# Kernel tuning notes

Measured on AMD Instinct MI355X. Metric: run time of the kernel, lower is better.

Reference implementation:

```python
import jax, jax.numpy as jnp
import numpy as np

VOCAB = 32000
HID = 1024
LAYERS = 2
BATCH = 16
SEQ = 256


def setup_inputs() -> dict:
    key = jax.random.key(0)
    ks = jax.random.split(key, 8)
    s = 1.0 / np.sqrt(HID)
    x = jax.random.randint(ks[0], (BATCH, SEQ), 0, VOCAB, dtype=jnp.int64)
    embed = jax.random.normal(ks[1], (VOCAB, HID), dtype=jnp.float32) * 0.02
    Wi = jax.random.uniform(ks[2], (LAYERS, HID, HID), jnp.float32, -s, s)
    bi = jax.random.uniform(ks[3], (LAYERS, HID), jnp.float32, -s, s)
    Wh = jax.random.uniform(ks[4], (LAYERS, HID, HID), jnp.float32, -s, s)
    bh = jax.random.uniform(ks[5], (LAYERS, HID), jnp.float32, -s, s)
    Wo = jax.random.uniform(ks[6], (VOCAB, HID), jnp.float32, -s, s)
    bo = jax.random.uniform(ks[7], (VOCAB,), jnp.float32, -s, s)
    return {"x": x, "embed": embed, "Wi": Wi, "bi": bi, "Wh": Wh, "bh": bh, "Wo": Wo, "bo": bo}


def reference(x, embed, Wi, bi, Wh, bh, Wo, bo):
    B, S = x.shape
    L, H, _ = Wi.shape
    emb = embed[x]                      # [B, S, H]
    emb_t = jnp.swapaxes(emb, 0, 1)     # [S, B, H]
    h0 = jnp.zeros((L, B, H), dtype=embed.dtype)

    def step(hidden, x_t):
        inp = x_t
        new_h = []
        for l in range(L):
            inp = jnp.tanh(inp @ Wi[l].T + bi[l] + hidden[l] @ Wh[l].T + bh[l])
            new_h.append(inp)
        hidden = jnp.stack(new_h)       # [L, B, H]
        return hidden, inp              # emit top-layer hidden per step

    hidden, tops = jax.lax.scan(step, h0, emb_t)   # tops: [S, B, H]
    # project all steps at once (same math as per-step fc_out)
    logits = jnp.einsum('sbh,vh->bsv', tops, Wo) + bo  # [B, S, V]
    return logits, hidden
```

## Files before the change

kernel.cpp:

```cpp
#include <hip/hip_runtime.h>
#include <cmath>
#include <cstdint>

#define VOCAB 32000
#define HID   1024
#define BATCH 16
#define SEQ   256
#define NL0   64
#define NL1   128
#define MASTER 192
#define NBLK  256
#define BH    (BATCH * HID)
#define NTILE_M 16
#define NTILE_N 125
#define NTILES  (NTILE_M * NTILE_N)

typedef __attribute__((ext_vector_type(8))) short short8;
typedef __attribute__((ext_vector_type(4))) float f32x4;

__device__ __forceinline__ ushort f2bf(float f) {
  uint u = __builtin_bit_cast(uint, f);
  return (ushort)((u + 0x7FFFu + ((u >> 16) & 1u)) >> 16);
}
__device__ __forceinline__ float bf2f(ushort h) {
  return __builtin_bit_cast(float, (uint)h << 16);
}

#define LOAD8(d, base)                                                        \
  asm volatile(                                                               \
    "global_load_dwordx4 %0, %8, off sc0 sc1\n\t"                             \
    "global_load_dwordx4 %1, %8, off offset:512 sc0 sc1\n\t"                  \
    "global_load_dwordx4 %2, %8, off offset:1024 sc0 sc1\n\t"                 \
    "global_load_dwordx4 %3, %8, off offset:1536 sc0 sc1\n\t"                 \
    "global_load_dwordx4 %4, %8, off offset:2048 sc0 sc1\n\t"                 \
    "global_load_dwordx4 %5, %8, off offset:2560 sc0 sc1\n\t"                 \
    "global_load_dwordx4 %6, %8, off offset:3072 sc0 sc1\n\t"                 \
    "global_load_dwordx4 %7, %8, off offset:3584 sc0 sc1"                     \
    : "=&v"(d[0]), "=&v"(d[1]), "=&v"(d[2]), "=&v"(d[3]),                     \
      "=&v"(d[4]), "=&v"(d[5]), "=&v"(d[6]), "=&v"(d[7])                      \
    : "v"(base) : "memory")

#define WAIT8(d)                                                              \
  asm volatile("s_waitcnt vmcnt(0)"                                           \
    : "+v"(d[0]), "+v"(d[1]), "+v"(d[2]), "+v"(d[3]),                         \
      "+v"(d[4]), "+v"(d[5]), "+v"(d[6]), "+v"(d[7]) :: "memory")

__device__ __forceinline__ void st_coherent(float* p, float v) {
  asm volatile("global_store_dword %0, %1, off sc0 sc1" :: "v"(p), "v"(v) : "memory");
}
__device__ __forceinline__ int ld_rlx(const int* p) {
  return __hip_atomic_load(p, __ATOMIC_RELAXED, __HIP_MEMORY_SCOPE_AGENT);
}
__device__ __forceinline__ void st_rlx(int* p, int v) {
  __hip_atomic_store(p, v, __ATOMIC_RELAXED, __HIP_MEMORY_SCOPE_AGENT);
}

__global__ __launch_bounds__(256) void pre0_gemm(
    const int* __restrict__ x, const float* __restrict__ embed,
    const float* __restrict__ Wi0, const float* __restrict__ bi0,
    const float* __restrict__ bh0, float* __restrict__ pre)
{
  __shared__ float As[32][132];
  __shared__ float Bs[32][132];
  const int tid  = threadIdx.x;
  const int n0   = blockIdx.x * 128;
  const int m0   = blockIdx.y * 128;
  const int lrow = tid >> 3, lkq = tid & 7;
  const int ty   = tid >> 4, tx  = tid & 15;

  const float* arow[4];
#pragma unroll
  for (int q = 0; q < 4; ++q) {
    int m = m0 + lrow + 32 * q;
    int t = m >> 4, b = m & 15;
    arow[q] = embed + (size_t)x[b * SEQ + t] * HID;
  }
  const float* brow = Wi0 + (size_t)(n0 + lrow) * HID;

  float acc[8][8];
#pragma unroll
  for (int i = 0; i < 8; ++i)
#pragma unroll
    for (int j = 0; j < 8; ++j) acc[i][j] = 0.f;

  for (int kt = 0; kt < HID; kt += 32) {
    float4 av[4], bv[4];
#pragma unroll
    for (int q = 0; q < 4; ++q) {
      av[q] = *(const float4*)(arow[q] + kt + lkq * 4);
      bv[q] = *(const float4*)(brow + (size_t)(32 * q) * HID + kt + lkq * 4);
    }
    __syncthreads();
#pragma unroll
    for (int q = 0; q < 4; ++q) {
      int r = lrow + 32 * q;
      As[lkq*4+0][r] = av[q].x; As[lkq*4+1][r] = av[q].y;
      As[lkq*4+2][r] = av[q].z; As[lkq*4+3][r] = av[q].w;
      Bs[lkq*4+0][r] = bv[q].x; Bs[lkq*4+1][r] = bv[q].y;
      Bs[lkq*4+2][r] = bv[q].z; Bs[lkq*4+3][r] = bv[q].w;
    }
    __syncthreads();
#pragma unroll
    for (int kk = 0; kk < 32; ++kk) {
      float4 a0 = *(const float4*)&As[kk][ty * 8];
      float4 a1 = *(const float4*)&As[kk][ty * 8 + 4];
      float4 b0 = *(const float4*)&Bs[kk][tx * 8];
      float4 b1 = *(const float4*)&Bs[kk][tx * 8 + 4];
      float a[8] = {a0.x,a0.y,a0.z,a0.w,a1.x,a1.y,a1.z,a1.w};
      float b[8] = {b0.x,b0.y,b0.z,b0.w,b1.x,b1.y,b1.z,b1.w};
#pragma unroll
      for (int i = 0; i < 8; ++i)
#pragma unroll
        for (int j = 0; j < 8; ++j) acc[i][j] = fmaf(a[i], b[j], acc[i][j]);
    }
  }

#pragma unroll
  for (int i = 0; i < 8; ++i) {
    int m = m0 + ty * 8 + i;
    float* o = pre + (size_t)m * HID + n0 + tx * 8;
#pragma unroll
    for (int j = 0; j < 8; ++j) {
      int n = n0 + tx * 8 + j;
      o[j] = acc[i][j] + bi0[n] + bh0[n];
    }
  }
}

__global__ __launch_bounds__(512) void rnn_scan(
    const float* __restrict__ Wi, const float* __restrict__ Wh,
    const float* __restrict__ bi, const float* __restrict__ bh,
    const float* __restrict__ pre0, float* __restrict__ h0ring,
    float* __restrict__ h1g, float* __restrict__ tops,
    const float* __restrict__ Wo, const float* __restrict__ bo,
    float* __restrict__ out, int* __restrict__ bar)
{
  __shared__ __align__(16) char pool[139328];
  __shared__ int tkt_s;
  const int tid = threadIdx.x;
  const int blk = blockIdx.x;
  int* go0    = bar + 12 * 32;
  int* go1    = bar + 13 * 32;
  int* ticket = bar + 14 * 32;

  auto proj_tiles = [&]() {
    ushort* Ahi = (ushort*)pool;
    ushort* Alo = Ahi + 16384;
    ushort* Bs  = Alo + 16384;
    const int lane = tid & 63, wv = tid >> 6;
    const int wm = wv & 3, wn = wv >> 2;
    const int sr = tid >> 4;
    const int sk = (tid & 15) * 4;
    for (;;) {
      if (tid == 0)
        tkt_s = __hip_atomic_fetch_add(ticket, 1, __ATOMIC_RELAXED,
                                       __HIP_MEMORY_SCOPE_AGENT);
      __syncthreads();
      const int T = tkt_s;
      if (T >= NTILES) break;
      const int mt = T / NTILE_N, nt = T % NTILE_N;
      if (tid == 0) {
        int need = 16 * (mt + 1); if (need > SEQ) need = SEQ;
        while (ld_rlx(go1) < need) __builtin_amdgcn_s_sleep(2);
      }
      __syncthreads();
      const int m0 = mt * 256, n0 = nt * 256;

      f32x4 acc[4][8];
#pragma unroll
      for (int i = 0; i < 4; ++i)
#pragma unroll
        for (int j = 0; j < 8; ++j) acc[i][j] = (f32x4)0.f;

      for (int kt = 0; kt < HID; kt += 64) {
        __syncthreads();
#pragma unroll
        for (int p = 0; p < 8; ++p) {
          int r = sr + 32 * p;
          float4 v = *(const float4*)(tops + (size_t)(m0 + r) * HID + kt + sk);
          float f[4] = {v.x, v.y, v.z, v.w};
          ushort hi[4], lo[4];
#pragma unroll
          for (int c = 0; c < 4; ++c) {
            hi[c] = f2bf(f[c]);
            lo[c] = f2bf(f[c] - bf2f(hi[c]));
          }
          uint off = (uint)(r * 128 + sk * 2) ^ (uint)((r & 7) << 4);
          *(ushort4*)((char*)Ahi + off) = make_ushort4(hi[0], hi[1], hi[2], hi[3]);
          *(ushort4*)((char*)Alo + off) = make_ushort4(lo[0], lo[1], lo[2], lo[3]);
        }
#pragma unroll
        for (int p = 0; p < 8; ++p) {
          int r = sr + 32 * p;
          float4 v = *(const float4*)(Wo + (size_t)(n0 + r) * HID + kt + sk);
          uint off = (uint)(r * 128 + sk * 2) ^ (uint)((r & 7) << 4);
          *(ushort4*)((char*)Bs + off) =
              make_ushort4(f2bf(v.x), f2bf(v.y), f2bf(v.z), f2bf(v.w));
        }
        __syncthreads();

        const int fr = lane & 15, kg = lane >> 4;
#pragma unroll
        for (int kk = 0; kk < 2; ++kk) {
          short8 bf[8], ah[4], al[4];
#pragma unroll
          for (int nf = 0; nf < 8; ++nf) {
            int row = wn * 128 + nf * 16 + fr;
            uint off = (uint)(row * 128 + kk * 64 + kg * 16) ^ (uint)((row & 7) << 4);
            bf[nf] = *(const short8*)((const char*)Bs + off);
          }
#pragma unroll
          for (int mf = 0; mf < 4; ++mf) {
            int row = wm * 64 + mf * 16 + fr;
            uint off = (uint)(row * 128 + kk * 64 + kg * 16) ^ (uint)((row & 7) << 4);
            ah[mf] = *(const short8*)((const char*)Ahi + off);
            al[mf] = *(const short8*)((const char*)Alo + off);
          }
#pragma unroll
          for (int mf = 0; mf < 4; ++mf)
#pragma unroll
            for (int nf = 0; nf < 8; ++nf) {
              acc[mf][nf] = __builtin_amdgcn_mfma_f32_16x16x32_bf16(
                  ah[mf], bf[nf], acc[mf][nf], 0, 0, 0);
              acc[mf][nf] = __builtin_amdgcn_mfma_f32_16x16x32_bf16(
                  al[mf], bf[nf], acc[mf][nf], 0, 0, 0);
            }
        }
      }

      const int fr = lane & 15, rg = lane >> 4;
#pragma unroll
      for (int mf = 0; mf < 4; ++mf)
#pragma unroll
        for (int nf = 0; nf < 8; ++nf) {
          int n = n0 + wn * 128 + nf * 16 + fr;
          float bb = bo[n];
#pragma unroll
          for (int j = 0; j < 4; ++j) {
            int m = m0 + wm * 64 + mf * 16 + rg * 4 + j;
            int orow = (m & 15) * 256 + (m >> 4);
            out[(size_t)orow * VOCAB + n] = acc[mf][nf][j] + bb;
          }
        }
    }
  };

  if (blk >= MASTER) {
    if (blk == MASTER && tid == 0) {
      int e0 = 0, e1 = 0;
      while (e0 < SEQ || e1 < SEQ) {
        int s0 = 0, s1 = 0;
#pragma unroll
        for (int i = 0; i < 4; ++i) s0 += ld_rlx(bar + i * 32);
#pragma unroll
        for (int i = 0; i < 8; ++i) s1 += ld_rlx(bar + (4 + i) * 32);
        int n0 = s0 >> 6;
        int n1 = s1 >> 7;
        if (n0 > e0) { e0 = n0; st_rlx(go0, e0); }
        if (n1 > e1) { e1 = n1; st_rlx(go1, e1); }
      }
    }
    proj_tiles();
    return;
  }

  float* wT   = (float*)pool;
  float* hT   = wT + 16384;
  float* part = hT + 16384;
  float* bias = part + 2048;

  const bool isL0 = (blk < NL0);

  if (isL0) {
    const int j = blk;
#pragma unroll
    for (int p = 0; p < 8; ++p) {
      int idx = tid + 512 * p;
      int r = idx >> 8, kq = idx & 255;
      float4 v = *(const float4*)(Wh + ((size_t)(16 * j + r)) * HID + 4 * kq);
      wT[(4*kq+0)*16 + r] = v.x; wT[(4*kq+1)*16 + r] = v.y;
      wT[(4*kq+2)*16 + r] = v.z; wT[(4*kq+3)*16 + r] = v.w;
    }
  } else {
    const int j = blk - NL0;
#pragma unroll
    for (int p = 0; p < 8; ++p) {
      int idx = tid + 512 * p;
      int half = idx >> 11;
      int id2 = idx & 2047;
      int r = id2 >> 8, kq = id2 & 255;
      const float* W = (half ? Wh : Wi) + (size_t)HID * HID;
      float4 v = *(const float4*)(W + ((size_t)(8 * j + r)) * HID + 4 * kq);
      int kb = half * 1024 + 4 * kq;
      wT[(kb+0)*8 + r] = v.x; wT[(kb+1)*8 + r] = v.y;
      wT[(kb+2)*8 + r] = v.z; wT[(kb+3)*8 + r] = v.w;
    }
    if (tid < 8) bias[tid] = bi[HID + 8 * j + tid] + bh[HID + 8 * j + tid];
  }
  __syncthreads();

  const int sb  = tid & 15;
  const int skq = tid >> 4;
  auto hbase = [&](const float* src) {
    return (const float*)((const char*)src + sb * 4096 + skq * 16);
  };
  auto stage_write = [&](const f32x4* d) {
#pragma unroll
    for (int p = 0; p < 8; ++p) {
      int kq = skq + 32 * p;
#pragma unroll
      for (int c = 0; c < 4; ++c) hT[(4*kq+c)*16 + sb] = d[p][c];
    }
  };

  if (isL0) {
    const int bq = tid & 3, rq = (tid >> 2) & 3, ks = tid >> 4;
    for (int u = 0; u < SEQ; ++u) {
      float myPre = 0.f;
      if (tid < 256)
        myPre = pre0[((size_t)u * BATCH + (tid >> 4)) * HID + 16 * blk + (tid & 15)];

      if (tid == 0) {
        while (ld_rlx(go0) < u) __builtin_amdgcn_s_sleep(1);
        const int need = u - 7;
        if (need > 0)
          while (ld_rlx(go1) < need) __builtin_amdgcn_s_sleep(1);
      }
      __syncthreads();

      f32x4 r0[8];
      LOAD8(r0, hbase(h0ring + ((u - 1) & 7) * BH));
      WAIT8(r0);
      stage_write(r0);
      __syncthreads();

      float acc[4][4] = {{0.f}};
#pragma unroll 4
      for (int i = 0; i < 32; ++i) {
        int k = ks + 32 * i;
        float4 hv = *(const float4*)&hT[k * 16 + 4 * bq];
        float4 wv = *(const float4*)&wT[k * 16 + 4 * rq];
        float hb[4] = {hv.x, hv.y, hv.z, hv.w};
        float wr[4] = {wv.x, wv.y, wv.z, wv.w};
#pragma unroll
        for (int b_ = 0; b_ < 4; ++b_)
#pragma unroll
          for (int rj = 0; rj < 4; ++rj)
            acc[b_][rj] = fmaf(hb[b_], wr[rj], acc[b_][rj]);
      }
#pragma unroll
      for (int b_ = 0; b_ < 4; ++b_)
#pragma unroll
        for (int rj = 0; rj < 4; ++rj) {
          float v = acc[b_][rj];
          v += __shfl_xor(v, 16); v += __shfl_xor(v, 32);
          acc[b_][rj] = v;
        }
      const int w = tid >> 6;
      if ((tid & 63) < 16) {
#pragma unroll
        for (int b_ = 0; b_ < 4; ++b_)
#pragma unroll
          for (int rj = 0; rj < 4; ++rj)
            part[w * 256 + (4*bq + b_) * 16 + 4*rq + rj] = acc[b_][rj];
      }
      __syncthreads();
      if (tid < 256) {
        int b = tid >> 4, r = tid & 15;
        float s = myPre;
#pragma unroll
        for (int w2 = 0; w2 < 8; ++w2) s += part[w2 * 256 + b * 16 + r];
        st_coherent(h0ring + (u & 7) * BH + (size_t)b * HID + 16 * blk + r, tanhf(s));
      }
      asm volatile("s_waitcnt vmcnt(0)" ::: "memory");
      __syncthreads();
      if (tid == 0)
        __hip_atomic_fetch_add(bar + (blk & 3) * 32, 1,
                               __ATOMIC_RELAXED, __HIP_MEMORY_SCOPE_AGENT);
    }
  } else {
    const int bq = tid & 3, rq = (tid >> 2) & 1, ks = tid >> 3;
    for (int t = 0; t < SEQ; ++t) {
      if (tid == 0)
        while (ld_rlx(go0) < t + 1) __builtin_amdgcn_s_sleep(1);
      __syncthreads();

      f32x4 r0[8];
      LOAD8(r0, hbase(h0ring + (t & 7) * BH));
      WAIT8(r0);
      stage_write(r0);
      __syncthreads();

      float acc[4][4] = {{0.f}};
#pragma unroll 4
      for (int i = 0; i < 16; ++i) {
        int k = ks + 64 * i;
        float4 hv = *(const float4*)&hT[k * 16 + 4 * bq];
        float4 wv = *(const float4*)&wT[k * 8 + 4 * rq];
        float hb[4] = {hv.x, hv.y, hv.z, hv.w};
        float wr[4] = {wv.x, wv.y, wv.z, wv.w};
#pragma unroll
        for (int b_ = 0; b_ < 4; ++b_)
#pragma unroll
          for (int rj = 0; rj < 4; ++rj)
            acc[b_][rj] = fmaf(hb[b_], wr[rj], acc[b_][rj]);
      }

      if (tid == 0 && t)
        while (ld_rlx(go1) < t) __builtin_amdgcn_s_sleep(1);
      __syncthreads();

      f32x4 r1[8];
      LOAD8(r1, hbase(h1g + ((t - 1) & 1) * BH));
      WAIT8(r1);
      stage_write(r1);
      __syncthreads();

#pragma unroll 4
      for (int i = 0; i < 16; ++i) {
        int k = ks + 64 * i;
        float4 hv = *(const float4*)&hT[k * 16 + 4 * bq];
        float4 wv = *(const float4*)&wT[(1024 + k) * 8 + 4 * rq];
        float hb[4] = {hv.x, hv.y, hv.z, hv.w};
        float wr[4] = {wv.x, wv.y, wv.z, wv.w};
#pragma unroll
        for (int b_ = 0; b_ < 4; ++b_)
#pragma unroll
          for (int rj = 0; rj < 4; ++rj)
            acc[b_][rj] = fmaf(hb[b_], wr[rj], acc[b_][rj]);
      }
#pragma unroll
      for (int b_ = 0; b_ < 4; ++b_)
#pragma unroll
        for (int rj = 0; rj < 4; ++rj) {
          float v = acc[b_][rj];
          v += __shfl_xor(v, 8); v += __shfl_xor(v, 16); v += __shfl_xor(v, 32);
          acc[b_][rj] = v;
        }
      const int w = tid >> 6;
      if ((tid & 63) < 8) {
#pragma unroll
        for (int b_ = 0; b_ < 4; ++b_)
#pragma unroll
          for (int rj = 0; rj < 4; ++rj)
            part[w * 128 + (4*bq + b_) * 8 + 4*rq + rj] = acc[b_][rj];
      }
      __syncthreads();
      if (tid < 128) {
        int b = tid >> 3, r = tid & 7;
        float s = bias[r];
#pragma unroll
        for (int w2 = 0; w2 < 8; ++w2) s += part[w2 * 128 + b * 8 + r];
        int R = 8 * (blk - NL0) + r;
        float v = tanhf(s);
        st_coherent(&tops[((size_t)t * BATCH + b) * HID + R], v);
        st_coherent(h1g + (t & 1) * BH + (size_t)b * HID + R, v);
      }
      asm volatile("s_waitcnt vmcnt(0)" ::: "memory");
      __syncthreads();
      if (tid == 0)
        __hip_atomic_fetch_add(bar + (4 + (blk & 7)) * 32, 1,
                               __ATOMIC_RELAXED, __HIP_MEMORY_SCOPE_AGENT);
    }
  }

  __syncthreads();
  proj_tiles();
}

__global__ void copy_hidden(const float* __restrict__ h0ring,
                            const float* __restrict__ tops,
                            float* __restrict__ outh)
{
  int i = blockIdx.x * 256 + threadIdx.x;
  int l = i >> 14, rem = i & 16383;
  outh[i] = (l == 0) ? h0ring[7 * BH + rem]
                     : tops[(size_t)(SEQ - 1) * BH + rem];
}

extern "C" void kernel_launch(void* const* d_in, const int* in_sizes, int n_in,
                              void* d_out, int out_size, void* d_ws, size_t ws_size,
                              hipStream_t stream)
{
  const int*   x     = (const int*)d_in[0];
  const float* embed = (const float*)d_in[1];
  const float* Wi    = (const float*)d_in[2];
  const float* bi    = (const float*)d_in[3];
  const float* Wh    = (const float*)d_in[4];
  const float* bh    = (const float*)d_in[5];
  const float* Wo    = (const float*)d_in[6];
  const float* bo    = (const float*)d_in[7];
  float* out = (float*)d_out;

  char* ws = (char*)d_ws;
  float* pre0   = (float*)(ws);
  float* tops   = (float*)(ws + (16u << 20));
  float* h0ring = (float*)(ws + (32u << 20));
  float* h1g    = (float*)(ws + (32u << 20) + 524288);
  int*   bar    = (int*)  (ws + (32u << 20) + 655360);

  hipMemsetAsync(h0ring, 0, 655360 + 4096, stream);

  pre0_gemm<<<dim3(8, 32), dim3(256), 0, stream>>>(x, embed, Wi, bi, bh, pre0);

  void* args[] = { (void*)&Wi, (void*)&Wh, (void*)&bi, (void*)&bh,
                   (void*)&pre0, (void*)&h0ring, (void*)&h1g, (void*)&tops,
                   (void*)&Wo, (void*)&bo, (void*)&out, (void*)&bar };
  hipLaunchCooperativeKernel((void*)rnn_scan, dim3(NBLK), dim3(512), args, 0, stream);

  copy_hidden<<<dim3(128), dim3(256), 0, stream>>>(
      h0ring, tops, out + (size_t)BATCH * SEQ * VOCAB);
}
```

Measured before the change: 2.801 ms.

## Pre-split tops into bf16 hi/lo, pre-convert Wo, replicate go flags

The layer-1 producer now writes each top hidden state as bf16 hi/lo halves directly, so projection tiles load ready bf16 operands instead of converting fp32 per tile. A separate kernel converts Wo to bf16 once per call into workspace (used only if the workspace is large enough), which halves Wo traffic in the projection loop and removes the repeated conversion across the 16 M-tiles. The go0/go1 progress flags are replicated across 8 cache lines to spread polling contention. The cost is an extra launch with a full Wo read and write, plus two 16-bit stores per output in the scan.

```diff
diff --git a/kernel.cpp b/kernel.cpp
--- a/kernel.cpp
+++ b/kernel.cpp
@@ -48,6 +48,9 @@
 __device__ __forceinline__ void st_coherent(float* p, float v) {
   asm volatile("global_store_dword %0, %1, off sc0 sc1" :: "v"(p), "v"(v) : "memory");
 }
+__device__ __forceinline__ void st_coherent_u16(ushort* p, ushort v) {
+  asm volatile("global_store_short %0, %1, off sc0 sc1" :: "v"(p), "v"((uint)v) : "memory");
+}
 __device__ __forceinline__ int ld_rlx(const int* p) {
   return __hip_atomic_load(p, __ATOMIC_RELAXED, __HIP_MEMORY_SCOPE_AGENT);
 }
@@ -127,21 +130,40 @@
   }
 }
 
+__global__ __launch_bounds__(256) void wo_conv(
+    const float* __restrict__ Wo, ushort* __restrict__ WoH)
+{
+  const size_t total = (size_t)VOCAB * HID;
+  for (size_t i = ((size_t)blockIdx.x * 256 + threadIdx.x) * 8; i < total;
+       i += (size_t)gridDim.x * 256 * 8) {
+    float4 v0 = *(const float4*)(Wo + i);
+    float4 v1 = *(const float4*)(Wo + i + 4);
+    short8 w;
+    w[0] = (short)f2bf(v0.x); w[1] = (short)f2bf(v0.y);
+    w[2] = (short)f2bf(v0.z); w[3] = (short)f2bf(v0.w);
+    w[4] = (short)f2bf(v1.x); w[5] = (short)f2bf(v1.y);
+    w[6] = (short)f2bf(v1.z); w[7] = (short)f2bf(v1.w);
+    *(short8*)(WoH + i) = w;
+  }
+}
+
 __global__ __launch_bounds__(512) void rnn_scan(
     const float* __restrict__ Wi, const float* __restrict__ Wh,
     const float* __restrict__ bi, const float* __restrict__ bh,
     const float* __restrict__ pre0, float* __restrict__ h0ring,
-    float* __restrict__ h1g, float* __restrict__ tops,
-    const float* __restrict__ Wo, const float* __restrict__ bo,
+    float* __restrict__ h1g, ushort* __restrict__ topsHi,
+    ushort* __restrict__ topsLo, const float* __restrict__ Wo,
+    const ushort* __restrict__ WoH, const float* __restrict__ bo,
     float* __restrict__ out, int* __restrict__ bar)
 {
   __shared__ __align__(16) char pool[139328];
   __shared__ int tkt_s;
   const int tid = threadIdx.x;
   const int blk = blockIdx.x;
-  int* go0    = bar + 12 * 32;
-  int* go1    = bar + 13 * 32;
-  int* ticket = bar + 14 * 32;
+  const int rep = (blk & 7) * 32;
+  int* go0r = bar + 12 * 32 + rep;
+  int* go1r = bar + 20 * 32 + rep;
+  int* ticket = bar + 28 * 32;
 
   auto proj_tiles = [&]() {
     ushort* Ahi = (ushort*)pool;
@@ -149,8 +171,8 @@
     ushort* Bs  = Alo + 16384;
     const int lane = tid & 63, wv = tid >> 6;
     const int wm = wv & 3, wn = wv >> 2;
-    const int sr = tid >> 4;
-    const int sk = (tid & 15) * 4;
+    const int sr8 = tid >> 3;
+    const int sk8 = (tid & 7) * 8;
     for (;;) {
       if (tid == 0)
         tkt_s = __hip_atomic_fetch_add(ticket, 1, __ATOMIC_RELAXED,
@@ -160,8 +182,8 @@
       if (T >= NTILES) break;
       const int mt = T / NTILE_N, nt = T % NTILE_N;
       if (tid == 0) {
-        int need = 16 * (mt + 1); if (need > SEQ) need = SEQ;
-        while (ld_rlx(go1) < need) __builtin_amdgcn_s_sleep(2);
+        const int need = 16 * (mt + 1);
+        while (ld_rlx(go1r) < need) __builtin_amdgcn_s_sleep(4);
       }
       __syncthreads();
       const int m0 = mt * 256, n0 = nt * 256;
@@ -175,27 +197,26 @@
       for (int kt = 0; kt < HID; kt += 64) {
         __syncthreads();
 #pragma unroll
-        for (int p = 0; p < 8; ++p) {
-          int r = sr + 32 * p;
-          float4 v = *(const float4*)(tops + (size_t)(m0 + r) * HID + kt + sk);
-          float f[4] = {v.x, v.y, v.z, v.w};
-          ushort hi[4], lo[4];
-#pragma unroll
-          for (int c = 0; c < 4; ++c) {
-            hi[c] = f2bf(f[c]);
-            lo[c] = f2bf(f[c] - bf2f(hi[c]));
+        for (int p = 0; p < 4; ++p) {
+          int r = sr8 + 64 * p;
+          uint off = (uint)(r * 128 + sk8 * 2) ^ (uint)((r & 7) << 4);
+          *(short8*)((char*)Ahi + off) =
+              *(const short8*)(topsHi + (size_t)(m0 + r) * HID + kt + sk8);
+          *(short8*)((char*)Alo + off) =
+              *(const short8*)(topsLo + (size_t)(m0 + r) * HID + kt + sk8);
+          if (WoH) {
+            *(short8*)((char*)Bs + off) =
+                *(const short8*)(WoH + (size_t)(n0 + r) * HID + kt + sk8);
+          } else {
+            float4 v0 = *(const float4*)(Wo + (size_t)(n0 + r) * HID + kt + sk8);
+            float4 v1 = *(const float4*)(Wo + (size_t)(n0 + r) * HID + kt + sk8 + 4);
+            short8 w;
+            w[0] = (short)f2bf(v0.x); w[1] = (short)f2bf(v0.y);
+            w[2] = (short)f2bf(v0.z); w[3] = (short)f2bf(v0.w);
+            w[4] = (short)f2bf(v1.x); w[5] = (short)f2bf(v1.y);
+            w[6] = (short)f2bf(v1.z); w[7] = (short)f2bf(v1.w);
+            *(short8*)((char*)Bs + off) = w;
           }
-          uint off = (uint)(r * 128 + sk * 2) ^ (uint)((r & 7) << 4);
-          *(ushort4*)((char*)Ahi + off) = make_ushort4(hi[0], hi[1], hi[2], hi[3]);
-          *(ushort4*)((char*)Alo + off) = make_ushort4(lo[0], lo[1], lo[2], lo[3]);
-        }
-#pragma unroll
-        for (int p = 0; p < 8; ++p) {
-          int r = sr + 32 * p;
-          float4 v = *(const float4*)(Wo + (size_t)(n0 + r) * HID + kt + sk);
-          uint off = (uint)(r * 128 + sk * 2) ^ (uint)((r & 7) << 4);
-          *(ushort4*)((char*)Bs + off) =
-              make_ushort4(f2bf(v.x), f2bf(v.y), f2bf(v.z), f2bf(v.w));
         }
         __syncthreads();
 
@@ -256,8 +277,16 @@
         for (int i = 0; i < 8; ++i) s1 += ld_rlx(bar + (4 + i) * 32);
         int n0 = s0 >> 6;
         int n1 = s1 >> 7;
-        if (n0 > e0) { e0 = n0; st_rlx(go0, e0); }
-        if (n1 > e1) { e1 = n1; st_rlx(go1, e1); }
+        if (n0 > e0) {
+          e0 = n0;
+#pragma unroll
+          for (int i = 0; i < 8; ++i) st_rlx(bar + (12 + i) * 32, e0);
+        }
+        if (n1 > e1) {
+          e1 = n1;
+#pragma unroll
+          for (int i = 0; i < 8; ++i) st_rlx(bar + (20 + i) * 32, e1);
+        }
       }
     }
     proj_tiles();
@@ -321,10 +350,10 @@
         myPre = pre0[((size_t)u * BATCH + (tid >> 4)) * HID + 16 * blk + (tid & 15)];
 
       if (tid == 0) {
-        while (ld_rlx(go0) < u) __builtin_amdgcn_s_sleep(1);
+        while (ld_rlx(go0r) < u) __builtin_amdgcn_s_sleep(1);
         const int need = u - 7;
         if (need > 0)
-          while (ld_rlx(go1) < need) __builtin_amdgcn_s_sleep(1);
+          while (ld_rlx(go1r) < need) __builtin_amdgcn_s_sleep(1);
       }
       __syncthreads();
 
@@ -382,7 +411,7 @@
     const int bq = tid & 3, rq = (tid >> 2) & 1, ks = tid >> 3;
     for (int t = 0; t < SEQ; ++t) {
       if (tid == 0)
-        while (ld_rlx(go0) < t + 1) __builtin_amdgcn_s_sleep(1);
+        while (ld_rlx(go0r) < t + 1) __builtin_amdgcn_s_sleep(1);
       __syncthreads();
 
       f32x4 r0[8];
@@ -407,7 +436,7 @@
       }
 
       if (tid == 0 && t)
-        while (ld_rlx(go1) < t) __builtin_amdgcn_s_sleep(1);
+        while (ld_rlx(go1r) < t) __builtin_amdgcn_s_sleep(1);
       __syncthreads();
 
       f32x4 r1[8];
@@ -453,7 +482,11 @@
         for (int w2 = 0; w2 < 8; ++w2) s += part[w2 * 128 + b * 8 + r];
         int R = 8 * (blk - NL0) + r;
         float v = tanhf(s);
-        st_coherent(&tops[((size_t)t * BATCH + b) * HID + R], v);
+        ushort hi = f2bf(v);
+        ushort lo = f2bf(v - bf2f(hi));
+        size_t mi = ((size_t)t * BATCH + b) * HID + R;
+        st_coherent_u16(topsHi + mi, hi);
+        st_coherent_u16(topsLo + mi, lo);
         st_coherent(h1g + (t & 1) * BH + (size_t)b * HID + R, v);
       }
       asm volatile("s_waitcnt vmcnt(0)" ::: "memory");
@@ -469,13 +502,18 @@
 }
 
 __global__ void copy_hidden(const float* __restrict__ h0ring,
-                            const float* __restrict__ tops,
+                            const ushort* __restrict__ topsHi,
+                            const ushort* __restrict__ topsLo,
                             float* __restrict__ outh)
 {
   int i = blockIdx.x * 256 + threadIdx.x;
   int l = i >> 14, rem = i & 16383;
-  outh[i] = (l == 0) ? h0ring[7 * BH + rem]
-                     : tops[(size_t)(SEQ - 1) * BH + rem];
+  if (l == 0) {
+    outh[i] = h0ring[7 * BH + rem];
+  } else {
+    size_t mi = (size_t)(SEQ - 1) * BH + rem;
+    outh[i] = bf2f(topsHi[mi]) + bf2f(topsLo[mi]);
+  }
 }
 
 extern "C" void kernel_launch(void* const* d_in, const int* in_sizes, int n_in,
@@ -493,21 +531,29 @@
   float* out = (float*)d_out;
 
   char* ws = (char*)d_ws;
-  float* pre0   = (float*)(ws);
-  float* tops   = (float*)(ws + (16u << 20));
-  float* h0ring = (float*)(ws + (32u << 20));
-  float* h1g    = (float*)(ws + (32u << 20) + 524288);
-  int*   bar    = (int*)  (ws + (32u << 20) + 655360);
-
-  hipMemsetAsync(h0ring, 0, 655360 + 4096, stream);
+  float*  pre0   = (float*) (ws);
+  ushort* topsHi = (ushort*)(ws + (16u << 20));
+  ushort* topsLo = (ushort*)(ws + (24u << 20));
+  float*  h0ring = (float*) (ws + (32u << 20));
+  float*  h1g    = (float*) (ws + (32u << 20) + 524288);
+  int*    bar    = (int*)   (ws + (32u << 20) + 655360);
+  ushort* WoH    = (ushort*)(ws + (33u << 20));
+  const size_t need_woh = (33ull << 20) + (size_t)VOCAB * HID * 2;
+  const bool useWoH = ws_size >= need_woh;
+
+  hipMemsetAsync(h0ring, 0, 659456, stream);
 
   pre0_gemm<<<dim3(8, 32), dim3(256), 0, stream>>>(x, embed, Wi, bi, bh, pre0);
-
+  if (useWoH)
+    wo_conv<<<dim3(2048), dim3(256), 0, stream>>>(Wo, WoH);
+
+  const ushort* WoHArg = useWoH ? WoH : (const ushort*)nullptr;
   void* args[] = { (void*)&Wi, (void*)&Wh, (void*)&bi, (void*)&bh,
-                   (void*)&pre0, (void*)&h0ring, (void*)&h1g, (void*)&tops,
-                   (void*)&Wo, (void*)&bo, (void*)&out, (void*)&bar };
+                   (void*)&pre0, (void*)&h0ring, (void*)&h1g,
+                   (void*)&topsHi, (void*)&topsLo, (void*)&Wo,
+                   (void*)&WoHArg, (void*)&bo, (void*)&out, (void*)&bar };
   hipLaunchCooperativeKernel((void*)rnn_scan, dim3(NBLK), dim3(512), args, 0, stream);
 
   copy_hidden<<<dim3(128), dim3(256), 0, stream>>>(
-      h0ring, tops, out + (size_t)BATCH * SEQ * VOCAB);
-}
+      h0ring, topsHi, topsLo, out + (size_t)BATCH * SEQ * VOCAB);
+}
```

Result: faster. 2.333 ms (-16.7%).
